# Optimization experiments

Measured on AMD Instinct MI355X. Metric: run time of the kernel, lower is better.

The kernel has to match this reference:

```python
import jax, jax.numpy as jnp
import numpy as np

D_MODEL = 512
N_EXPERTS = 8
HIDDEN = D_MODEL * 4
EPS = 1e-10

def setup_inputs() -> dict:
    key = jax.random.key(0)
    ks = jax.random.split(key, 8)
    B, N = 4, 2048
    T = B * N
    x = jax.random.normal(ks[0], (B, N, D_MODEL), dtype=jnp.float32)
    u = jax.random.uniform(ks[1], (T, N_EXPERTS), dtype=jnp.float32, minval=1e-6, maxval=1.0)
    s_in = 1.0 / np.sqrt(D_MODEL)
    s_h = 1.0 / np.sqrt(HIDDEN)
    router_w = jax.random.uniform(ks[2], (D_MODEL, N_EXPERTS), jnp.float32, -s_in, s_in)
    router_b = jax.random.uniform(ks[3], (N_EXPERTS,), jnp.float32, -s_in, s_in)
    w1 = jax.random.uniform(ks[4], (N_EXPERTS, D_MODEL, HIDDEN), jnp.float32, -s_in, s_in)
    b1 = jax.random.uniform(ks[5], (N_EXPERTS, HIDDEN), jnp.float32, -s_in, s_in)
    w2 = jax.random.uniform(ks[6], (N_EXPERTS, HIDDEN, D_MODEL), jnp.float32, -s_h, s_h)
    b2 = jax.random.uniform(ks[7], (N_EXPERTS, D_MODEL), jnp.float32, -s_h, s_h)
    return {"x": x, "u": u, "router_w": router_w, "router_b": router_b,
            "w1": w1, "b1": b1, "w2": w2, "b2": b2}

def reference(x, u, router_w, router_b, w1, b1, w2, b2):
    B, N, d = x.shape
    x_flat = x.reshape(-1, d)  # (T, d)
    logits = x_flat @ router_w + router_b  # (T, E)
    # Gumbel-softmax, tau=1.0, hard=True (straight-through)
    g = -jnp.log(-jnp.log(u) + EPS)
    y_soft = jax.nn.softmax(logits + g, axis=-1)
    idx = jnp.argmax(y_soft, axis=-1)
    hard = jax.nn.one_hot(idx, logits.shape[-1], dtype=y_soft.dtype)
    weights = hard - jax.lax.stop_gradient(y_soft) + y_soft  # (T, E)
    # aux load-balancing loss
    probs = jax.nn.softmax(logits, axis=-1)
    importance = probs.sum(axis=0) / jnp.maximum(jnp.float32(logits.shape[0]), 1.0)
    target = 1.0 / logits.shape[-1]
    aux_loss = jnp.mean((importance - target) ** 2)
    # all-expert dense compute then weighted combine
    h = jax.nn.gelu(jnp.einsum('td,edh->eth', x_flat, w1) + b1[:, None, :], approximate=False)
    expert_outputs = jnp.einsum('eth,ehd->etd', h, w2) + b2[:, None, :]  # (E, T, d)
    output = jnp.einsum('te,etd->td', weights, expert_outputs)
    return output.reshape(B, N, d), aux_loss
```

## Files before the change

### kernel.cpp

```cpp
#include <hip/hip_runtime.h>
#include <stdint.h>
#include <math.h>

#define NUM_TOK 8192
#define DM 512
#define NE 8
#define NH 2048
#define MAX_TILES 72
#define NBLK 32

typedef float f32x4 __attribute__((ext_vector_type(4)));
typedef __bf16 bf16x8 __attribute__((ext_vector_type(8)));

#define WS_COUNTS   0
#define WS_OFFSETS  64
#define WS_IMP      96
#define WS_TILE_E   128
#define WS_TILE_R0  416
#define WS_EXP      704
#define WS_WTOK     33472
#define WS_PERM     66240
#define WS_XG       99008
#define WS_H        8618688
#define WS_W1T      42697408
#define WS_W2T      59474624
#define WS_PROBS    WS_XG
#define WS_RANK     WS_H
#define WS_BHIST    (WS_H + 32768)
#define WS_BBASE    (WS_H + 33792)

__device__ __forceinline__ uint16_t f2bf(float f) {
  union { float f; uint32_t u; } c; c.f = f;
  return (uint16_t)((c.u + 0x7FFFu + ((c.u >> 16) & 1u)) >> 16);
}

__device__ __forceinline__ float gelu_fast(float v) {
  float z = 1.5957691216f * v * (1.0f + 0.044715f * v * v);
  float em = __expf(-z);
  return v / (1.0f + em);
}

__device__ __forceinline__ void gload_lds16(const void* g, void* l) {
  __builtin_amdgcn_global_load_lds(
      (const __attribute__((address_space(1))) uint32_t*)g,
      (__attribute__((address_space(3))) uint32_t*)l, 16, 0, 0);
}

#define WAIT_BARRIER(N) asm volatile("s_waitcnt vmcnt(" #N ")\ns_barrier" ::: "memory")
#define RAW_BARRIER()   asm volatile("s_barrier" ::: "memory")

__global__ __launch_bounds__(256) void k_router(
    const float* __restrict__ x, const float* __restrict__ u,
    const float* __restrict__ rw, const float* __restrict__ rb,
    int* __restrict__ expert_of, float* __restrict__ wtok,
    float* __restrict__ probs)
{
  int wv = threadIdx.x >> 6, lane = threadIdx.x & 63;
  int t = blockIdx.x * 4 + wv;

  const float4* xr = (const float4*)(x + (size_t)t * DM + lane * 8);
  float4 xa = xr[0], xb = xr[1];
  float xs[8] = {xa.x, xa.y, xa.z, xa.w, xb.x, xb.y, xb.z, xb.w};

  double acc[NE];
  #pragma unroll
  for (int e = 0; e < NE; ++e) acc[e] = 0.0;
  #pragma unroll
  for (int j = 0; j < 8; ++j) {
    const float4* rr = (const float4*)(rw + (size_t)(lane * 8 + j) * NE);
    float4 r0 = rr[0], r1 = rr[1];
    double xv = (double)xs[j];
    acc[0] += xv * (double)r0.x; acc[1] += xv * (double)r0.y;
    acc[2] += xv * (double)r0.z; acc[3] += xv * (double)r0.w;
    acc[4] += xv * (double)r1.x; acc[5] += xv * (double)r1.y;
    acc[6] += xv * (double)r1.z; acc[7] += xv * (double)r1.w;
  }
  #pragma unroll
  for (int m = 1; m < 64; m <<= 1) {
    #pragma unroll
    for (int e = 0; e < NE; ++e) acc[e] += __shfl_xor(acc[e], m, 64);
  }
  double lg[NE];
  #pragma unroll
  for (int e = 0; e < NE; ++e) lg[e] = acc[e] + (double)rb[e];

  int le = lane & 7;
  double lgE = le == 0 ? lg[0] : le == 1 ? lg[1] : le == 2 ? lg[2] : le == 3 ? lg[3]
             : le == 4 ? lg[4] : le == 5 ? lg[5] : le == 6 ? lg[6] : lg[7];

  double yE = -1e300;
  if (lane < 8) {
    double uv = (double)u[(size_t)t * NE + lane];
    double g = -log(-log(uv) + 1e-10);
    yE = lgE + g;
  }
  double ymax = yE;
  #pragma unroll
  for (int m = 1; m < 8; m <<= 1) ymax = fmax(ymax, __shfl_xor(ymax, m, 64));
  double ex = (lane < 8) ? exp(yE - ymax) : 0.0;
  double s = ex;
  #pragma unroll
  for (int m = 1; m < 8; m <<= 1) s += __shfl_xor(s, m, 64);
  double p = 1.0 / s;
  unsigned long long mk = __ballot(lane < 8 && yE == ymax);
  int sel = __ffsll(mk) - 1;

  double lm = lgE;
  #pragma unroll
  for (int m = 1; m < 8; m <<= 1) lm = fmax(lm, __shfl_xor(lm, m, 64));
  double pr = exp(lgE - lm);
  double ssum = pr;
  #pragma unroll
  for (int m = 1; m < 8; m <<= 1) ssum += __shfl_xor(ssum, m, 64);

  if (lane < 8) probs[(size_t)t * NE + lane] = (float)(pr / ssum);
  if (lane == 0) {
    expert_of[t] = sel;
    wtok[t] = (float)((1.0 - p) + p);
  }
}

__global__ __launch_bounds__(256) void k_postroute(
    const int* __restrict__ expert_of, const float* __restrict__ probs,
    int* __restrict__ rank_local, int* __restrict__ block_hist,
    float* __restrict__ imp)
{
  __shared__ int whist[4][8];
  __shared__ float simp[4][8];
  int tid = threadIdx.x, lane = tid & 63, wid = tid >> 6;
  int t = blockIdx.x * 256 + tid;
  int sel = expert_of[t];

  int cnt[8]; int lrank = 0;
  unsigned long long below = (1ull << lane) - 1ull;
  #pragma unroll
  for (int e = 0; e < 8; ++e) {
    unsigned long long m = __ballot(sel == e);
    cnt[e] = (int)__popcll(m);
    if (e == sel) lrank = (int)__popcll(m & below);
  }
  if (lane == 0) {
    #pragma unroll
    for (int e = 0; e < 8; ++e) whist[wid][e] = cnt[e];
  }

  const float4* pp = (const float4*)(probs + (size_t)t * NE);
  float4 pa = pp[0], pb = pp[1];
  float ps[8] = {pa.x, pa.y, pa.z, pa.w, pb.x, pb.y, pb.z, pb.w};
  #pragma unroll
  for (int j = 0; j < 8; ++j) {
    float v = ps[j];
    #pragma unroll
    for (int m = 1; m < 64; m <<= 1) v += __shfl_xor(v, m, 64);
    if (lane == 0) simp[wid][j] = v;
  }
  __syncthreads();

  int base = 0;
  #pragma unroll
  for (int w = 0; w < 4; ++w) if (w < wid) base += whist[w][sel];
  rank_local[t] = base + lrank;

  if (tid < 8) {
    int c = whist[0][tid] + whist[1][tid] + whist[2][tid] + whist[3][tid];
    block_hist[blockIdx.x * 8 + tid] = c;
    float sv = simp[0][tid] + simp[1][tid] + simp[2][tid] + simp[3][tid];
    atomicAdd(&imp[tid], sv);
  }
}

__global__ __launch_bounds__(256) void k_offsets(
    const int* __restrict__ block_hist, const float* __restrict__ imp,
    int* __restrict__ counts, int* __restrict__ offsets,
    int* __restrict__ block_base, float* __restrict__ aux_out,
    int* __restrict__ tile_e, int* __restrict__ tile_r0)
{
  __shared__ int sh[NBLK * 8];
  __shared__ int scnt[8];
  __shared__ int soff[8];
  __shared__ float simp[8];
  int tid = threadIdx.x;

  sh[tid] = block_hist[tid];
  if (tid < 8) simp[tid] = imp[tid];
  __syncthreads();

  if (tid < 8) {
    int c = 0;
    #pragma unroll
    for (int b = 0; b < NBLK; ++b) c += sh[b * 8 + tid];
    scnt[tid] = c;
    counts[tid] = c;
  }
  __syncthreads();

  if (tid == 0) {
    int o = 0;
    #pragma unroll
    for (int e = 0; e < NE; ++e) { soff[e] = o; offsets[e] = o; o += scnt[e]; }
    float a = 0.0f;
    #pragma unroll
    for (int e = 0; e < NE; ++e) {
      float dv = simp[e] / 8192.0f - 0.125f;
      a += dv * dv;
    }
    aux_out[0] = a / 8.0f;
    int nt = 0;
    for (int e = 0; e < NE; ++e) {
      int ntile = (scnt[e] + 127) >> 7;
      for (int j = 0; j < ntile; ++j) { tile_e[nt] = e; tile_r0[nt] = soff[e] + j * 128; ++nt; }
    }
    for (int i = nt; i < MAX_TILES; ++i) { tile_e[i] = -1; tile_r0[i] = 0; }
  }
  __syncthreads();

  int b = tid >> 3, e = tid & 7;
  int run = soff[e];
  for (int bp = 0; bp < b; ++bp) run += sh[bp * 8 + e];
  block_base[tid] = run;
}

__global__ __launch_bounds__(256) void k_scatter2(
    const int* __restrict__ expert_of, const int* __restrict__ rank_local,
    const int* __restrict__ block_base, int* __restrict__ perm)
{
  int t = blockIdx.x * 256 + threadIdx.x;
  int e = expert_of[t];
  perm[block_base[blockIdx.x * 8 + e] + rank_local[t]] = t;
}

__global__ __launch_bounds__(64) void k_gather(
    const float* __restrict__ x, const int* __restrict__ perm, uint16_t* __restrict__ Xg)
{
  int r = blockIdx.x;
  int lane = threadIdx.x;
  int t = perm[r];
  const float4* src = (const float4*)(x + (size_t)t * DM);
  float4 a = src[lane * 2];
  float4 b = src[lane * 2 + 1];
  uint32_t p0 = (uint32_t)f2bf(a.x) | ((uint32_t)f2bf(a.y) << 16);
  uint32_t p1 = (uint32_t)f2bf(a.z) | ((uint32_t)f2bf(a.w) << 16);
  uint32_t p2 = (uint32_t)f2bf(b.x) | ((uint32_t)f2bf(b.y) << 16);
  uint32_t p3 = (uint32_t)f2bf(b.z) | ((uint32_t)f2bf(b.w) << 16);
  uint4 v = make_uint4(p0, p1, p2, p3);
  ((uint4*)(Xg + (size_t)r * DM))[lane] = v;
}

__global__ __launch_bounds__(256) void k_transpose_bf16(
    const float* __restrict__ src, uint16_t* __restrict__ dst, int K, int N)
{
  __shared__ float T[64][65];
  int e = blockIdx.z;
  const float* s = src + (size_t)e * K * N;
  uint16_t* d = dst + (size_t)e * K * N;
  int n0 = blockIdx.x * 64, k0 = blockIdx.y * 64;
  int tid = threadIdx.x;
  int tr = tid >> 4;
  int tc = (tid & 15) * 4;
  #pragma unroll
  for (int p = 0; p < 4; ++p) {
    int k = tr + p * 16;
    float4 v = *(const float4*)(s + (size_t)(k0 + k) * N + n0 + tc);
    T[k][tc] = v.x; T[k][tc + 1] = v.y; T[k][tc + 2] = v.z; T[k][tc + 3] = v.w;
  }
  __syncthreads();
  #pragma unroll
  for (int p = 0; p < 2; ++p) {
    int slot = p * 256 + tid;
    int n = slot >> 3;
    int c = (slot & 7) * 8;
    uint16_t tmp[8];
    #pragma unroll
    for (int j = 0; j < 8; ++j) tmp[j] = f2bf(T[c + j][n]);
    *(uint4*)(d + (size_t)(n0 + n) * K + k0 + c) = *(uint4*)tmp;
  }
}

__device__ __forceinline__ void mfma_128x128(
    const uint16_t* Asb, const uint16_t* Bsb, f32x4 (&acc)[4][4],
    int wm, int wn, int l16, int quad)
{
  #pragma unroll
  for (int ks = 0; ks < 2; ++ks) {
    bf16x8 a[4], b[4];
    #pragma unroll
    for (int mi = 0; mi < 4; ++mi) {
      int row = wm * 64 + mi * 16 + l16;
      a[mi] = *(const bf16x8*)(Asb + row * 64 + (((ks * 4 + quad) ^ (l16 & 7)) * 8));
    }
    #pragma unroll
    for (int ni = 0; ni < 4; ++ni) {
      int row = wn * 64 + ni * 16 + l16;
      b[ni] = *(const bf16x8*)(Bsb + row * 64 + (((ks * 4 + quad) ^ (l16 & 7)) * 8));
    }
    #pragma unroll
    for (int mi = 0; mi < 4; ++mi)
      #pragma unroll
      for (int ni = 0; ni < 4; ++ni)
        acc[mi][ni] = __builtin_amdgcn_mfma_f32_16x16x32_bf16(a[mi], b[ni], acc[mi][ni], 0, 0, 0);
  }
}

__global__ __launch_bounds__(256) void k_ffn1(
    const uint16_t* __restrict__ Xg, const uint16_t* __restrict__ w1t,
    const float* __restrict__ b1,
    const int* __restrict__ offsets, const int* __restrict__ counts,
    const int* __restrict__ tile_e, const int* __restrict__ tile_r0,
    uint16_t* __restrict__ hbuf)
{
  int e = tile_e[blockIdx.x];
  if (e < 0) return;
  int row0 = tile_r0[blockIdx.x];
  int row_end = offsets[e] + counts[e];
  int n0 = blockIdx.y * 128;
  const uint16_t* Bt = w1t + (size_t)e * DM * NH;

  __shared__ uint16_t As[2][128 * 64];
  __shared__ uint16_t Bs[2][128 * 64];

  int tid = threadIdx.x;
  int lane = tid & 63, wid = tid >> 6;
  int wm = wid >> 1, wn = wid & 1;
  int l16 = lane & 15, quad = lane >> 4;

  int lrow = lane >> 3;
  int lsw  = (lane & 7) ^ lrow;
  const uint16_t *ga[4], *gb[4];
  int lo[4];
  #pragma unroll
  for (int j = 0; j < 4; ++j) {
    int r = wid * 32 + j * 8;
    ga[j] = Xg + (size_t)(row0 + r + lrow) * DM + lsw * 8;
    gb[j] = Bt + (size_t)(n0 + r + lrow) * DM + lsw * 8;
    lo[j] = r * 64;
  }

  #define FFN1_ISSUE(B) do { \
    _Pragma("unroll") for (int j = 0; j < 4; ++j) { gload_lds16(ga[j], As[B] + lo[j]); ga[j] += 64; } \
    _Pragma("unroll") for (int j = 0; j < 4; ++j) { gload_lds16(gb[j], Bs[B] + lo[j]); gb[j] += 64; } \
  } while (0)

  f32x4 acc[4][4] = {};

  FFN1_ISSUE(0);
  FFN1_ISSUE(1);
  #pragma unroll 2
  for (int k = 0; k < 8; ++k) {
    if (k < 7) WAIT_BARRIER(8); else WAIT_BARRIER(0);
    int b = k & 1;
    mfma_128x128(As[b], Bs[b], acc, wm, wn, l16, quad);
    RAW_BARRIER();
    if (k < 6) { if (b) FFN1_ISSUE(1); else FFN1_ISSUE(0); }
  }

  #pragma unroll
  for (int ni = 0; ni < 4; ++ni) {
    int col = n0 + wn * 64 + ni * 16 + l16;
    float bv = b1[e * NH + col];
    #pragma unroll
    for (int mi = 0; mi < 4; ++mi) {
      int rbase = wm * 64 + mi * 16 + quad * 4;
      #pragma unroll
      for (int r = 0; r < 4; ++r) {
        int grow = row0 + rbase + r;
        if (grow < row_end) {
          float v = acc[mi][ni][r] + bv;
          hbuf[(size_t)grow * NH + col] = f2bf(gelu_fast(v));
        }
      }
    }
  }
}

__global__ __launch_bounds__(256) void k_ffn2(
    const uint16_t* __restrict__ hbuf, const uint16_t* __restrict__ w2t,
    const float* __restrict__ b2,
    const int* __restrict__ offsets, const int* __restrict__ counts,
    const int* __restrict__ tile_e, const int* __restrict__ tile_r0,
    const int* __restrict__ perm, const float* __restrict__ wtok,
    float* __restrict__ out)
{
  int e = tile_e[blockIdx.x];
  if (e < 0) return;
  int row0 = tile_r0[blockIdx.x];
  int row_end = offsets[e] + counts[e];
  int n0 = blockIdx.y * 64;
  const uint16_t* Bt = w2t + (size_t)e * NH * DM;

  __shared__ uint16_t As[2][128 * 64];
  __shared__ uint16_t Bs[2][64 * 64];

  int tid = threadIdx.x;
  int lane = tid & 63, wid = tid >> 6;
  int wm = wid >> 1, wn = wid & 1;
  int l16 = lane & 15, quad = lane >> 4;

  int lrow = lane >> 3;
  int lsw  = (lane & 7) ^ lrow;
  const uint16_t *ga[4], *gb[2];
  int loa[4], lob[2];
  #pragma unroll
  for (int j = 0; j < 4; ++j) {
    int r = wid * 32 + j * 8;
    ga[j] = hbuf + (size_t)(row0 + r + lrow) * NH + lsw * 8;
    loa[j] = r * 64;
  }
  #pragma unroll
  for (int j = 0; j < 2; ++j) {
    int r = wid * 16 + j * 8;
    gb[j] = Bt + (size_t)(n0 + r + lrow) * NH + lsw * 8;
    lob[j] = r * 64;
  }

  #define FFN2_ISSUE(B) do { \
    _Pragma("unroll") for (int j = 0; j < 4; ++j) { gload_lds16(ga[j], As[B] + loa[j]); ga[j] += 64; } \
    _Pragma("unroll") for (int j = 0; j < 2; ++j) { gload_lds16(gb[j], Bs[B] + lob[j]); gb[j] += 64; } \
  } while (0)

  f32x4 acc[4][2] = {};

  FFN2_ISSUE(0);
  FFN2_ISSUE(1);
  #pragma unroll 2
  for (int k = 0; k < 32; ++k) {
    if (k < 31) WAIT_BARRIER(6); else WAIT_BARRIER(0);
    int b = k & 1;
    const uint16_t* Ab = As[b];
    const uint16_t* Bb = Bs[b];
    #pragma unroll
    for (int ks = 0; ks < 2; ++ks) {
      bf16x8 a[4], bb[2];
      #pragma unroll
      for (int mi = 0; mi < 4; ++mi) {
        int row = wm * 64 + mi * 16 + l16;
        a[mi] = *(const bf16x8*)(Ab + row * 64 + (((ks * 4 + quad) ^ (l16 & 7)) * 8));
      }
      #pragma unroll
      for (int ni = 0; ni < 2; ++ni) {
        int row = wn * 32 + ni * 16 + l16;
        bb[ni] = *(const bf16x8*)(Bb + row * 64 + (((ks * 4 + quad) ^ (l16 & 7)) * 8));
      }
      #pragma unroll
      for (int mi = 0; mi < 4; ++mi)
        #pragma unroll
        for (int ni = 0; ni < 2; ++ni)
          acc[mi][ni] = __builtin_amdgcn_mfma_f32_16x16x32_bf16(a[mi], bb[ni], acc[mi][ni], 0, 0, 0);
    }
    RAW_BARRIER();
    if (k < 30) { if (b) FFN2_ISSUE(1); else FFN2_ISSUE(0); }
  }

  #pragma unroll
  for (int ni = 0; ni < 2; ++ni) {
    int col = n0 + wn * 32 + ni * 16 + l16;
    float bv = b2[e * DM + col];
    #pragma unroll
    for (int mi = 0; mi < 4; ++mi) {
      int rbase = wm * 64 + mi * 16 + quad * 4;
      #pragma unroll
      for (int r = 0; r < 4; ++r) {
        int grow = row0 + rbase + r;
        if (grow < row_end) {
          int tk = perm[grow];
          float wt = wtok[tk];
          out[(size_t)tk * DM + col] = (acc[mi][ni][r] + bv) * wt;
        }
      }
    }
  }
}

extern "C" void kernel_launch(void* const* d_in, const int* in_sizes, int n_in,
                              void* d_out, int out_size, void* d_ws, size_t ws_size,
                              hipStream_t stream)
{
  const float* x  = (const float*)d_in[0];
  const float* u  = (const float*)d_in[1];
  const float* rw = (const float*)d_in[2];
  const float* rb = (const float*)d_in[3];
  const float* w1 = (const float*)d_in[4];
  const float* b1 = (const float*)d_in[5];
  const float* w2 = (const float*)d_in[6];
  const float* b2 = (const float*)d_in[7];
  float* out = (float*)d_out;

  char* ws = (char*)d_ws;
  int*      counts     = (int*)(ws + WS_COUNTS);
  int*      offsets    = (int*)(ws + WS_OFFSETS);
  float*    imp        = (float*)(ws + WS_IMP);
  int*      tile_e     = (int*)(ws + WS_TILE_E);
  int*      tile_r0    = (int*)(ws + WS_TILE_R0);
  int*      expert_of  = (int*)(ws + WS_EXP);
  float*    wtok       = (float*)(ws + WS_WTOK);
  int*      perm       = (int*)(ws + WS_PERM);
  float*    probs      = (float*)(ws + WS_PROBS);
  int*      rank_local = (int*)(ws + WS_RANK);
  int*      block_hist = (int*)(ws + WS_BHIST);
  int*      block_base = (int*)(ws + WS_BBASE);
  uint16_t* Xg         = (uint16_t*)(ws + WS_XG);
  uint16_t* hbuf       = (uint16_t*)(ws + WS_H);
  uint16_t* w1t        = (uint16_t*)(ws + WS_W1T);
  uint16_t* w2t        = (uint16_t*)(ws + WS_W2T);

  hipMemsetAsync(d_ws, 0, 128, stream);
  k_transpose_bf16<<<dim3(NH / 64, DM / 64, NE), 256, 0, stream>>>(w1, w1t, DM, NH);
  k_transpose_bf16<<<dim3(DM / 64, NH / 64, NE), 256, 0, stream>>>(w2, w2t, NH, DM);
  k_router<<<NUM_TOK / 4, 256, 0, stream>>>(x, u, rw, rb, expert_of, wtok, probs);
  k_postroute<<<NBLK, 256, 0, stream>>>(expert_of, probs, rank_local, block_hist, imp);
  k_offsets<<<1, 256, 0, stream>>>(block_hist, imp, counts, offsets, block_base,
                                   out + (size_t)NUM_TOK * DM, tile_e, tile_r0);
  k_scatter2<<<NBLK, 256, 0, stream>>>(expert_of, rank_local, block_base, perm);
  k_gather<<<NUM_TOK, 64, 0, stream>>>(x, perm, Xg);
  k_ffn1<<<dim3(MAX_TILES, 16), 256, 0, stream>>>(Xg, w1t, b1, offsets, counts, tile_e, tile_r0, hbuf);
  k_ffn2<<<dim3(MAX_TILES, 8), 256, 0, stream>>>(hbuf, w2t, b2, offsets, counts, tile_e, tile_r0, perm, wtok, out);
}
```

Before: 295.3 us.

## Remap FFN grids for XCD-aware locality and widen FFN2 tiles to 128x128

Both FFN kernels move to a 1D grid whose block index is remapped so that each of the 8 XCDs (blockIdx mod 8) gets a contiguous chunk of tile/column work. The goal is better L2 reuse of the expert weights and activations. FFN2 also grows its output tile from 128x64 to 128x128 and reuses the shared mfma_128x128 routine, which halves the block count and the redundant re-reads of hbuf. The trade-offs are more registers and LDS per block and fewer blocks, which could hurt occupancy and tail balance.

Result: no change. 291.6 us (-1.2%).

```diff
diff --git a/kernel.cpp b/kernel.cpp
--- a/kernel.cpp
+++ b/kernel.cpp
@@ -308,11 +308,14 @@
     const int* __restrict__ tile_e, const int* __restrict__ tile_r0,
     uint16_t* __restrict__ hbuf)
 {
-  int e = tile_e[blockIdx.x];
+  int w = (blockIdx.x & 7) * (MAX_TILES * 16 / 8) + (blockIdx.x >> 3);
+  int tile = w >> 4;
+  int cb = w & 15;
+  int e = tile_e[tile];
   if (e < 0) return;
-  int row0 = tile_r0[blockIdx.x];
+  int row0 = tile_r0[tile];
   int row_end = offsets[e] + counts[e];
-  int n0 = blockIdx.y * 128;
+  int n0 = cb * 128;
   const uint16_t* Bt = w1t + (size_t)e * DM * NH;
 
   __shared__ uint16_t As[2][128 * 64];
@@ -380,15 +383,18 @@
     const int* __restrict__ perm, const float* __restrict__ wtok,
     float* __restrict__ out)
 {
-  int e = tile_e[blockIdx.x];
+  int w = (blockIdx.x & 7) * (MAX_TILES * 4 / 8) + (blockIdx.x >> 3);
+  int tile = w >> 2;
+  int cb = w & 3;
+  int e = tile_e[tile];
   if (e < 0) return;
-  int row0 = tile_r0[blockIdx.x];
+  int row0 = tile_r0[tile];
   int row_end = offsets[e] + counts[e];
-  int n0 = blockIdx.y * 64;
+  int n0 = cb * 128;
   const uint16_t* Bt = w2t + (size_t)e * NH * DM;
 
   __shared__ uint16_t As[2][128 * 64];
-  __shared__ uint16_t Bs[2][64 * 64];
+  __shared__ uint16_t Bs[2][128 * 64];
 
   int tid = threadIdx.x;
   int lane = tid & 63, wid = tid >> 6;
@@ -397,62 +403,37 @@
 
   int lrow = lane >> 3;
   int lsw  = (lane & 7) ^ lrow;
-  const uint16_t *ga[4], *gb[2];
-  int loa[4], lob[2];
+  const uint16_t *ga[4], *gb[4];
+  int lo[4];
   #pragma unroll
   for (int j = 0; j < 4; ++j) {
     int r = wid * 32 + j * 8;
     ga[j] = hbuf + (size_t)(row0 + r + lrow) * NH + lsw * 8;
-    loa[j] = r * 64;
-  }
-  #pragma unroll
-  for (int j = 0; j < 2; ++j) {
-    int r = wid * 16 + j * 8;
     gb[j] = Bt + (size_t)(n0 + r + lrow) * NH + lsw * 8;
-    lob[j] = r * 64;
+    lo[j] = r * 64;
   }
 
   #define FFN2_ISSUE(B) do { \
-    _Pragma("unroll") for (int j = 0; j < 4; ++j) { gload_lds16(ga[j], As[B] + loa[j]); ga[j] += 64; } \
-    _Pragma("unroll") for (int j = 0; j < 2; ++j) { gload_lds16(gb[j], Bs[B] + lob[j]); gb[j] += 64; } \
+    _Pragma("unroll") for (int j = 0; j < 4; ++j) { gload_lds16(ga[j], As[B] + lo[j]); ga[j] += 64; } \
+    _Pragma("unroll") for (int j = 0; j < 4; ++j) { gload_lds16(gb[j], Bs[B] + lo[j]); gb[j] += 64; } \
   } while (0)
 
-  f32x4 acc[4][2] = {};
+  f32x4 acc[4][4] = {};
 
   FFN2_ISSUE(0);
   FFN2_ISSUE(1);
   #pragma unroll 2
   for (int k = 0; k < 32; ++k) {
-    if (k < 31) WAIT_BARRIER(6); else WAIT_BARRIER(0);
+    if (k < 31) WAIT_BARRIER(8); else WAIT_BARRIER(0);
     int b = k & 1;
-    const uint16_t* Ab = As[b];
-    const uint16_t* Bb = Bs[b];
-    #pragma unroll
-    for (int ks = 0; ks < 2; ++ks) {
-      bf16x8 a[4], bb[2];
-      #pragma unroll
-      for (int mi = 0; mi < 4; ++mi) {
-        int row = wm * 64 + mi * 16 + l16;
-        a[mi] = *(const bf16x8*)(Ab + row * 64 + (((ks * 4 + quad) ^ (l16 & 7)) * 8));
-      }
-      #pragma unroll
-      for (int ni = 0; ni < 2; ++ni) {
-        int row = wn * 32 + ni * 16 + l16;
-        bb[ni] = *(const bf16x8*)(Bb + row * 64 + (((ks * 4 + quad) ^ (l16 & 7)) * 8));
-      }
-      #pragma unroll
-      for (int mi = 0; mi < 4; ++mi)
-        #pragma unroll
-        for (int ni = 0; ni < 2; ++ni)
-          acc[mi][ni] = __builtin_amdgcn_mfma_f32_16x16x32_bf16(a[mi], bb[ni], acc[mi][ni], 0, 0, 0);
-    }
+    mfma_128x128(As[b], Bs[b], acc, wm, wn, l16, quad);
     RAW_BARRIER();
     if (k < 30) { if (b) FFN2_ISSUE(1); else FFN2_ISSUE(0); }
   }
 
   #pragma unroll
-  for (int ni = 0; ni < 2; ++ni) {
-    int col = n0 + wn * 32 + ni * 16 + l16;
+  for (int ni = 0; ni < 4; ++ni) {
+    int col = n0 + wn * 64 + ni * 16 + l16;
     float bv = b2[e * DM + col];
     #pragma unroll
     for (int mi = 0; mi < 4; ++mi) {
@@ -511,6 +492,6 @@
                                    out + (size_t)NUM_TOK * DM, tile_e, tile_r0);
   k_scatter2<<<NBLK, 256, 0, stream>>>(expert_of, rank_local, block_base, perm);
   k_gather<<<NUM_TOK, 64, 0, stream>>>(x, perm, Xg);
-  k_ffn1<<<dim3(MAX_TILES, 16), 256, 0, stream>>>(Xg, w1t, b1, offsets, counts, tile_e, tile_r0, hbuf);
-  k_ffn2<<<dim3(MAX_TILES, 8), 256, 0, stream>>>(hbuf, w2t, b2, offsets, counts, tile_e, tile_r0, perm, wtok, out);
-}
+  k_ffn1<<<dim3(MAX_TILES * 16), 256, 0, stream>>>(Xg, w1t, b1, offsets, counts, tile_e, tile_r0, hbuf);
+  k_ffn2<<<dim3(MAX_TILES * 4), 256, 0, stream>>>(hbuf, w2t, b2, offsets, counts, tile_e, tile_r0, perm, wtok, out);
+}
```

## Use 8-wave blocks in FFN GEMMs, remap grid for XCD locality, merge transposes

Applied to the files above, without the earlier changes.

Both expert GEMM kernels now run 512 threads (8 waves) per block, so each wave owns a smaller sub-tile and the block has more waves to hide latency. The 2D grid becomes a 1D grid remapped so that consecutive tiles sharing an expert's weights land on the same XCD, aiming to improve L2 reuse. The two weight-transpose launches are merged into one kernel to remove a launch. The trade-off is fewer MFMAs per LDS fragment load per wave, and possibly fewer resident blocks per CU.

New measurement: 261.5 us. 1.13x faster.

```diff
diff --git a/kernel.cpp b/kernel.cpp
--- a/kernel.cpp
+++ b/kernel.cpp
@@ -246,14 +246,20 @@
   ((uint4*)(Xg + (size_t)r * DM))[lane] = v;
 }
 
-__global__ __launch_bounds__(256) void k_transpose_bf16(
-    const float* __restrict__ src, uint16_t* __restrict__ dst, int K, int N)
+__global__ __launch_bounds__(256) void k_transpose_both(
+    const float* __restrict__ w1, const float* __restrict__ w2,
+    uint16_t* __restrict__ w1t, uint16_t* __restrict__ w2t)
 {
   __shared__ float T[64][65];
-  int e = blockIdx.z;
+  int id = blockIdx.x;
+  const float* src; uint16_t* dst; int K, N, nx, rid;
+  if (id < 2048) { src = w1; dst = w1t; K = DM; N = NH; nx = NH / 64; rid = id; }
+  else           { src = w2; dst = w2t; K = NH; N = DM; nx = DM / 64; rid = id - 2048; }
+  int e = rid >> 8;
+  int r = rid & 255;
+  int n0 = (r % nx) * 64, k0 = (r / nx) * 64;
   const float* s = src + (size_t)e * K * N;
   uint16_t* d = dst + (size_t)e * K * N;
-  int n0 = blockIdx.x * 64, k0 = blockIdx.y * 64;
   int tid = threadIdx.x;
   int tr = tid >> 4;
   int tc = (tid & 15) * 4;
@@ -276,43 +282,21 @@
   }
 }
 
-__device__ __forceinline__ void mfma_128x128(
-    const uint16_t* Asb, const uint16_t* Bsb, f32x4 (&acc)[4][4],
-    int wm, int wn, int l16, int quad)
-{
-  #pragma unroll
-  for (int ks = 0; ks < 2; ++ks) {
-    bf16x8 a[4], b[4];
-    #pragma unroll
-    for (int mi = 0; mi < 4; ++mi) {
-      int row = wm * 64 + mi * 16 + l16;
-      a[mi] = *(const bf16x8*)(Asb + row * 64 + (((ks * 4 + quad) ^ (l16 & 7)) * 8));
-    }
-    #pragma unroll
-    for (int ni = 0; ni < 4; ++ni) {
-      int row = wn * 64 + ni * 16 + l16;
-      b[ni] = *(const bf16x8*)(Bsb + row * 64 + (((ks * 4 + quad) ^ (l16 & 7)) * 8));
-    }
-    #pragma unroll
-    for (int mi = 0; mi < 4; ++mi)
-      #pragma unroll
-      for (int ni = 0; ni < 4; ++ni)
-        acc[mi][ni] = __builtin_amdgcn_mfma_f32_16x16x32_bf16(a[mi], b[ni], acc[mi][ni], 0, 0, 0);
-  }
-}
-
-__global__ __launch_bounds__(256) void k_ffn1(
+__global__ __launch_bounds__(512) void k_ffn1(
     const uint16_t* __restrict__ Xg, const uint16_t* __restrict__ w1t,
     const float* __restrict__ b1,
     const int* __restrict__ offsets, const int* __restrict__ counts,
     const int* __restrict__ tile_e, const int* __restrict__ tile_r0,
     uint16_t* __restrict__ hbuf)
 {
-  int e = tile_e[blockIdx.x];
+  int w = (blockIdx.x & 7) * (MAX_TILES * 16 / 8) + (blockIdx.x >> 3);
+  int tile = w >> 4;
+  int cb = w & 15;
+  int e = tile_e[tile];
   if (e < 0) return;
-  int row0 = tile_r0[blockIdx.x];
+  int row0 = tile_r0[tile];
   int row_end = offsets[e] + counts[e];
-  int n0 = blockIdx.y * 128;
+  int n0 = cb * 128;
   const uint16_t* Bt = w1t + (size_t)e * DM * NH;
 
   __shared__ uint16_t As[2][128 * 64];
@@ -320,42 +304,62 @@
 
   int tid = threadIdx.x;
   int lane = tid & 63, wid = tid >> 6;
-  int wm = wid >> 1, wn = wid & 1;
+  int wm = wid >> 2, wn = wid & 3;
   int l16 = lane & 15, quad = lane >> 4;
 
   int lrow = lane >> 3;
   int lsw  = (lane & 7) ^ lrow;
-  const uint16_t *ga[4], *gb[4];
-  int lo[4];
-  #pragma unroll
-  for (int j = 0; j < 4; ++j) {
-    int r = wid * 32 + j * 8;
+  const uint16_t *ga[2], *gb[2];
+  int lo[2];
+  #pragma unroll
+  for (int j = 0; j < 2; ++j) {
+    int r = wid * 16 + j * 8;
     ga[j] = Xg + (size_t)(row0 + r + lrow) * DM + lsw * 8;
     gb[j] = Bt + (size_t)(n0 + r + lrow) * DM + lsw * 8;
     lo[j] = r * 64;
   }
 
   #define FFN1_ISSUE(B) do { \
-    _Pragma("unroll") for (int j = 0; j < 4; ++j) { gload_lds16(ga[j], As[B] + lo[j]); ga[j] += 64; } \
-    _Pragma("unroll") for (int j = 0; j < 4; ++j) { gload_lds16(gb[j], Bs[B] + lo[j]); gb[j] += 64; } \
+    _Pragma("unroll") for (int j = 0; j < 2; ++j) { gload_lds16(ga[j], As[B] + lo[j]); ga[j] += 64; } \
+    _Pragma("unroll") for (int j = 0; j < 2; ++j) { gload_lds16(gb[j], Bs[B] + lo[j]); gb[j] += 64; } \
   } while (0)
 
-  f32x4 acc[4][4] = {};
+  f32x4 acc[4][2] = {};
 
   FFN1_ISSUE(0);
   FFN1_ISSUE(1);
   #pragma unroll 2
   for (int k = 0; k < 8; ++k) {
-    if (k < 7) WAIT_BARRIER(8); else WAIT_BARRIER(0);
+    if (k < 7) WAIT_BARRIER(4); else WAIT_BARRIER(0);
     int b = k & 1;
-    mfma_128x128(As[b], Bs[b], acc, wm, wn, l16, quad);
+    const uint16_t* Ab = As[b];
+    const uint16_t* Bb = Bs[b];
+    #pragma unroll
+    for (int ks = 0; ks < 2; ++ks) {
+      bf16x8 a[4], bb[2];
+      #pragma unroll
+      for (int mi = 0; mi < 4; ++mi) {
+        int row = wm * 64 + mi * 16 + l16;
+        a[mi] = *(const bf16x8*)(Ab + row * 64 + (((ks * 4 + quad) ^ (l16 & 7)) * 8));
+      }
+      #pragma unroll
+      for (int ni = 0; ni < 2; ++ni) {
+        int row = wn * 32 + ni * 16 + l16;
+        bb[ni] = *(const bf16x8*)(Bb + row * 64 + (((ks * 4 + quad) ^ (l16 & 7)) * 8));
+      }
+      #pragma unroll
+      for (int mi = 0; mi < 4; ++mi)
+        #pragma unroll
+        for (int ni = 0; ni < 2; ++ni)
+          acc[mi][ni] = __builtin_amdgcn_mfma_f32_16x16x32_bf16(a[mi], bb[ni], acc[mi][ni], 0, 0, 0);
+    }
     RAW_BARRIER();
     if (k < 6) { if (b) FFN1_ISSUE(1); else FFN1_ISSUE(0); }
   }
 
   #pragma unroll
-  for (int ni = 0; ni < 4; ++ni) {
-    int col = n0 + wn * 64 + ni * 16 + l16;
+  for (int ni = 0; ni < 2; ++ni) {
+    int col = n0 + wn * 32 + ni * 16 + l16;
     float bv = b1[e * NH + col];
     #pragma unroll
     for (int mi = 0; mi < 4; ++mi) {
@@ -372,7 +376,7 @@
   }
 }
 
-__global__ __launch_bounds__(256) void k_ffn2(
+__global__ __launch_bounds__(512) void k_ffn2(
     const uint16_t* __restrict__ hbuf, const uint16_t* __restrict__ w2t,
     const float* __restrict__ b2,
     const int* __restrict__ offsets, const int* __restrict__ counts,
@@ -380,11 +384,14 @@
     const int* __restrict__ perm, const float* __restrict__ wtok,
     float* __restrict__ out)
 {
-  int e = tile_e[blockIdx.x];
+  int w = (blockIdx.x & 7) * (MAX_TILES * 8 / 8) + (blockIdx.x >> 3);
+  int tile = w >> 3;
+  int cb = w & 7;
+  int e = tile_e[tile];
   if (e < 0) return;
-  int row0 = tile_r0[blockIdx.x];
+  int row0 = tile_r0[tile];
   int row_end = offsets[e] + counts[e];
-  int n0 = blockIdx.y * 64;
+  int n0 = cb * 64;
   const uint16_t* Bt = w2t + (size_t)e * NH * DM;
 
   __shared__ uint16_t As[2][128 * 64];
@@ -397,42 +404,41 @@
 
   int lrow = lane >> 3;
   int lsw  = (lane & 7) ^ lrow;
-  const uint16_t *ga[4], *gb[2];
-  int loa[4], lob[2];
-  #pragma unroll
-  for (int j = 0; j < 4; ++j) {
-    int r = wid * 32 + j * 8;
+  const uint16_t *ga[2], *gb;
+  int loa[2], lob;
+  #pragma unroll
+  for (int j = 0; j < 2; ++j) {
+    int r = wid * 16 + j * 8;
     ga[j] = hbuf + (size_t)(row0 + r + lrow) * NH + lsw * 8;
     loa[j] = r * 64;
   }
-  #pragma unroll
-  for (int j = 0; j < 2; ++j) {
-    int r = wid * 16 + j * 8;
-    gb[j] = Bt + (size_t)(n0 + r + lrow) * NH + lsw * 8;
-    lob[j] = r * 64;
+  {
+    int r = wid * 8;
+    gb = Bt + (size_t)(n0 + r + lrow) * NH + lsw * 8;
+    lob = r * 64;
   }
 
   #define FFN2_ISSUE(B) do { \
-    _Pragma("unroll") for (int j = 0; j < 4; ++j) { gload_lds16(ga[j], As[B] + loa[j]); ga[j] += 64; } \
-    _Pragma("unroll") for (int j = 0; j < 2; ++j) { gload_lds16(gb[j], Bs[B] + lob[j]); gb[j] += 64; } \
+    _Pragma("unroll") for (int j = 0; j < 2; ++j) { gload_lds16(ga[j], As[B] + loa[j]); ga[j] += 64; } \
+    gload_lds16(gb, Bs[B] + lob); gb += 64; \
   } while (0)
 
-  f32x4 acc[4][2] = {};
+  f32x4 acc[2][2] = {};
 
   FFN2_ISSUE(0);
   FFN2_ISSUE(1);
   #pragma unroll 2
   for (int k = 0; k < 32; ++k) {
-    if (k < 31) WAIT_BARRIER(6); else WAIT_BARRIER(0);
+    if (k < 31) WAIT_BARRIER(3); else WAIT_BARRIER(0);
     int b = k & 1;
     const uint16_t* Ab = As[b];
     const uint16_t* Bb = Bs[b];
     #pragma unroll
     for (int ks = 0; ks < 2; ++ks) {
-      bf16x8 a[4], bb[2];
-      #pragma unroll
-      for (int mi = 0; mi < 4; ++mi) {
-        int row = wm * 64 + mi * 16 + l16;
+      bf16x8 a[2], bb[2];
+      #pragma unroll
+      for (int mi = 0; mi < 2; ++mi) {
+        int row = wm * 32 + mi * 16 + l16;
         a[mi] = *(const bf16x8*)(Ab + row * 64 + (((ks * 4 + quad) ^ (l16 & 7)) * 8));
       }
       #pragma unroll
@@ -441,7 +447,7 @@
         bb[ni] = *(const bf16x8*)(Bb + row * 64 + (((ks * 4 + quad) ^ (l16 & 7)) * 8));
       }
       #pragma unroll
-      for (int mi = 0; mi < 4; ++mi)
+      for (int mi = 0; mi < 2; ++mi)
         #pragma unroll
         for (int ni = 0; ni < 2; ++ni)
           acc[mi][ni] = __builtin_amdgcn_mfma_f32_16x16x32_bf16(a[mi], bb[ni], acc[mi][ni], 0, 0, 0);
@@ -455,8 +461,8 @@
     int col = n0 + wn * 32 + ni * 16 + l16;
     float bv = b2[e * DM + col];
     #pragma unroll
-    for (int mi = 0; mi < 4; ++mi) {
-      int rbase = wm * 64 + mi * 16 + quad * 4;
+    for (int mi = 0; mi < 2; ++mi) {
+      int rbase = wm * 32 + mi * 16 + quad * 4;
       #pragma unroll
       for (int r = 0; r < 4; ++r) {
         int grow = row0 + rbase + r;
@@ -503,14 +509,13 @@
   uint16_t* w2t        = (uint16_t*)(ws + WS_W2T);
 
   hipMemsetAsync(d_ws, 0, 128, stream);
-  k_transpose_bf16<<<dim3(NH / 64, DM / 64, NE), 256, 0, stream>>>(w1, w1t, DM, NH);
-  k_transpose_bf16<<<dim3(DM / 64, NH / 64, NE), 256, 0, stream>>>(w2, w2t, NH, DM);
+  k_transpose_both<<<dim3(4096), 256, 0, stream>>>(w1, w2, w1t, w2t);
   k_router<<<NUM_TOK / 4, 256, 0, stream>>>(x, u, rw, rb, expert_of, wtok, probs);
   k_postroute<<<NBLK, 256, 0, stream>>>(expert_of, probs, rank_local, block_hist, imp);
   k_offsets<<<1, 256, 0, stream>>>(block_hist, imp, counts, offsets, block_base,
                                    out + (size_t)NUM_TOK * DM, tile_e, tile_r0);
   k_scatter2<<<NBLK, 256, 0, stream>>>(expert_of, rank_local, block_base, perm);
   k_gather<<<NUM_TOK, 64, 0, stream>>>(x, perm, Xg);
-  k_ffn1<<<dim3(MAX_TILES, 16), 256, 0, stream>>>(Xg, w1t, b1, offsets, counts, tile_e, tile_r0, hbuf);
-  k_ffn2<<<dim3(MAX_TILES, 8), 256, 0, stream>>>(hbuf, w2t, b2, offsets, counts, tile_e, tile_r0, perm, wtok, out);
-}
+  k_ffn1<<<dim3(MAX_TILES * 16), 512, 0, stream>>>(Xg, w1t, b1, offsets, counts, tile_e, tile_r0, hbuf);
+  k_ffn2<<<dim3(MAX_TILES * 8), 512, 0, stream>>>(hbuf, w2t, b2, offsets, counts, tile_e, tile_r0, perm, wtok, out);
+}
```
